# Kernel optimization log

Hardware: AMD Instinct MI355X
Metric: run time of the kernel (lower is better)

The kernel has to match this reference:

```python
import jax, jax.numpy as jnp
import numpy as np

B, T, D, E, I = 4, 2048, 2048, 8, 1024
TOP_K = 2
AUX_COEFF = 0.01


def setup_inputs() -> dict:
    key = jax.random.key(0)
    kx, kg, k1, k3, k2 = jax.random.split(key, 5)
    scale = 0.02
    x = jax.random.normal(kx, (B, T, D), dtype=jnp.float32)
    gate_w = jax.random.normal(kg, (E, D), dtype=jnp.float32) * scale   # nn.Linear weight [out,in]
    w1 = jax.random.normal(k1, (E, I, D), dtype=jnp.float32) * scale    # gate_proj per expert
    w3 = jax.random.normal(k3, (E, I, D), dtype=jnp.float32) * scale    # up_proj per expert
    w2 = jax.random.normal(k2, (E, D, I), dtype=jnp.float32) * scale    # down_proj per expert
    return {"x": x, "gate_w": gate_w, "w1": w1, "w3": w3, "w2": w2}


def reference(x, gate_w, w1, w3, w2):
    b, t, d = x.shape
    e = gate_w.shape[0]
    xf = x.reshape(b * t, d)                                   # [N, D]
    logits = xf @ gate_w.T                                     # [N, E]
    scores = jax.nn.softmax(logits, axis=-1)
    top_scores, top_idx = jax.lax.top_k(scores, TOP_K)         # [N, K]
    top_scores = top_scores / jnp.sum(top_scores, axis=-1, keepdims=True)
    # load-balancing aux loss (Switch Transformer)
    expert_mask = jax.nn.one_hot(top_idx, e, dtype=x.dtype).sum(axis=1)  # [N, E]
    f = expert_mask.mean(axis=0)
    p = scores.mean(axis=0)
    aux_loss = AUX_COEFF * e * jnp.sum(f * p)
    # dense all-expert SwiGLU (matches torch module's dense dispatch)
    h = jax.nn.silu(jnp.einsum('td,eid->tei', xf, w1)) * jnp.einsum('td,eid->tei', xf, w3)  # [N,E,I]
    expert_outs = jnp.einsum('tei,edi->ted', h, w2)            # [N, E, D]
    selected = jnp.take_along_axis(expert_outs, top_idx[:, :, None], axis=1)  # [N, K, D]
    out = jnp.sum(selected * top_scores[:, :, None], axis=1)   # [N, D]
    return out.reshape(b, t, d), aux_loss
```

## Files before the change

### kernel.cpp

```cpp
#include <hip/hip_runtime.h>
#include <hip/hip_bf16.h>

constexpr int kN = 8192;
constexpr int kD = 2048;
constexpr int kE = 8;
constexpr int kI = 1024;

typedef __bf16 bf16x8 __attribute__((ext_vector_type(8)));
typedef float  f32x16 __attribute__((ext_vector_type(16)));

constexpr size_t OFF_COUNTS = 0;
constexpr size_t OFF_PSUM   = 64;
constexpr size_t OFF_OFFS   = 128;
constexpr size_t OFF_CURSOR = 192;
constexpr size_t OFF_TOPE   = 256;
constexpr size_t OFF_TOPW   = OFF_TOPE + (size_t)kN * 8;
constexpr size_t OFF_SLOT   = OFF_TOPW + (size_t)kN * 8;
constexpr size_t OFF_TOK    = OFF_SLOT + (size_t)kN * 8;
constexpr size_t OFF_XG     = OFF_TOK + (size_t)kN * 8;
constexpr size_t OFF_W1B    = OFF_XG  + (size_t)2 * kN * kD * 2;
constexpr size_t OFF_W3B    = OFF_W1B + (size_t)kE * kI * kD * 2;
constexpr size_t OFF_W2B    = OFF_W3B + (size_t)kE * kI * kD * 2;
constexpr size_t OFF_H      = OFF_W2B + (size_t)kE * kD * kI * 2;
constexpr size_t OFF_O2     = OFF_XG;

typedef __attribute__((address_space(1))) const unsigned GU;
typedef __attribute__((address_space(3))) unsigned LU;
__device__ __forceinline__ void gload16(const void* g, void* l) {
    __builtin_amdgcn_global_load_lds((GU*)g, (LU*)l, 16, 0, 0);
}

__global__ __launch_bounds__(256) void convert3_kernel(
    const float* __restrict__ s0, const float* __restrict__ s1,
    const float* __restrict__ s2,
    __bf16* __restrict__ d0, __bf16* __restrict__ d1, __bf16* __restrict__ d2,
    int n8seg)
{
    const int seg = blockIdx.x >> 11;
    const int bid = blockIdx.x & 2047;
    const float* src = (seg == 0) ? s0 : (seg == 1) ? s1 : s2;
    __bf16*      dst = (seg == 0) ? d0 : (seg == 1) ? d1 : d2;
    int i = bid * 256 + threadIdx.x;
    const int stride = 2048 * 256;
    for (; i < n8seg; i += stride) {
        const float4* s = (const float4*)(src + (size_t)i * 8);
        float4 f0 = s[0], f1 = s[1];
        bf16x8 v;
        v[0]=(__bf16)f0.x; v[1]=(__bf16)f0.y; v[2]=(__bf16)f0.z; v[3]=(__bf16)f0.w;
        v[4]=(__bf16)f1.x; v[5]=(__bf16)f1.y; v[6]=(__bf16)f1.z; v[7]=(__bf16)f1.w;
        *(bf16x8*)(dst + (size_t)i * 8) = v;
    }
}

__global__ __launch_bounds__(256) void gate_kernel(
    const float* __restrict__ x, const float* __restrict__ gw,
    unsigned* __restrict__ counts, float* __restrict__ psum,
    int2* __restrict__ tope, float2* __restrict__ topw)
{
    const int tid  = threadIdx.x;
    const int lane = tid & 63;
    const int wv   = tid >> 6;
    const int t    = blockIdx.x * 4 + wv;

    const float* xr = x + (size_t)t * kD;
    float xv[32];
#pragma unroll
    for (int j = 0; j < 32; ++j) xv[j] = xr[lane + 64 * j];

    float s[8];
#pragma unroll
    for (int e = 0; e < 8; ++e) {
        const float* gr = gw + (size_t)e * kD;
        float a = 0.f;
#pragma unroll
        for (int j = 0; j < 32; ++j) a += xv[j] * gr[lane + 64 * j];
        s[e] = a;
    }
#pragma unroll
    for (int off = 32; off > 0; off >>= 1) {
#pragma unroll
        for (int e = 0; e < 8; ++e) s[e] += __shfl_xor(s[e], off, 64);
    }
    float mx = s[0];
#pragma unroll
    for (int e = 1; e < 8; ++e) mx = fmaxf(mx, s[e]);
    float p[8]; float sum = 0.f;
#pragma unroll
    for (int e = 0; e < 8; ++e) { p[e] = expf(s[e] - mx); sum += p[e]; }
    float inv = 1.f / sum;
#pragma unroll
    for (int e = 0; e < 8; ++e) p[e] *= inv;

    int e0 = 0; float p0 = p[0];
#pragma unroll
    for (int e = 1; e < 8; ++e) if (p[e] > p0) { p0 = p[e]; e0 = e; }
    int e1 = -1; float p1 = -1.f;
#pragma unroll
    for (int e = 0; e < 8; ++e) if (e != e0 && p[e] > p1) { p1 = p[e]; e1 = e; }
    float wn = 1.f / (p0 + p1);

    __shared__ float ps[4][8];
    __shared__ unsigned cnt[8];
    if (tid < 8) cnt[tid] = 0u;
    __syncthreads();
    if (lane == 0) {
#pragma unroll
        for (int e = 0; e < 8; ++e) ps[wv][e] = p[e];
        atomicAdd(&cnt[e0], 1u);
        atomicAdd(&cnt[e1], 1u);
        tope[t] = make_int2(e0, e1);
        topw[t] = make_float2(p0 * wn, p1 * wn);
    }
    __syncthreads();
    if (tid < 8) {
        atomicAdd(&psum[tid], ps[0][tid] + ps[1][tid] + ps[2][tid] + ps[3][tid]);
        if (cnt[tid]) atomicAdd(&counts[tid], cnt[tid]);
    }
}

__global__ void scan_kernel(const unsigned* __restrict__ counts,
                            const float* __restrict__ psum,
                            unsigned* __restrict__ offs,
                            unsigned* __restrict__ cursor,
                            float* __restrict__ out)
{
    if (threadIdx.x == 0) {
        unsigned off = 0;
        float a = 0.f;
        for (int e = 0; e < 8; ++e) {
            offs[e] = off; cursor[e] = off; off += counts[e];
            a += ((float)counts[e] / (float)kN) * (psum[e] / (float)kN);
        }
        out[(size_t)kN * kD] = 0.01f * (float)kE * a;
    }
}

__global__ __launch_bounds__(256) void scatter_kernel(
    const int2* __restrict__ tope,
    unsigned* __restrict__ cursor, int* __restrict__ tok,
    int2* __restrict__ slotmap)
{
    int t = blockIdx.x * 256 + threadIdx.x;
    int2 ee = tope[t];
    unsigned q0 = atomicAdd(&cursor[ee.x], 1u);
    tok[q0] = t;
    unsigned q1 = atomicAdd(&cursor[ee.y], 1u);
    tok[q1] = t;
    slotmap[t] = make_int2((int)q0, (int)q1);
}

__global__ __launch_bounds__(256) void gather_kernel(
    const float* __restrict__ x, const int* __restrict__ tok,
    __bf16* __restrict__ Xg)
{
    const int total = 2 * kN * (kD / 8);
    int i = blockIdx.x * 256 + threadIdx.x;
    const int stride = gridDim.x * 256;
    for (; i < total; i += stride) {
        const int slot = i >> 8;
        const int d8   = (i & 255) * 8;
        const float4* s = (const float4*)(x + (size_t)tok[slot] * kD + d8);
        float4 f0 = s[0], f1 = s[1];
        bf16x8 v;
        v[0]=(__bf16)f0.x; v[1]=(__bf16)f0.y; v[2]=(__bf16)f0.z; v[3]=(__bf16)f0.w;
        v[4]=(__bf16)f1.x; v[5]=(__bf16)f1.y; v[6]=(__bf16)f1.z; v[7]=(__bf16)f1.w;
        *(bf16x8*)(Xg + (size_t)slot * kD + d8) = v;
    }
}

__global__ __launch_bounds__(256) void ffn_h_kernel(
    const __bf16* __restrict__ Xg,
    const __bf16* __restrict__ w1b, const __bf16* __restrict__ w3b,
    const unsigned* __restrict__ counts, const unsigned* __restrict__ offs,
    __bf16* __restrict__ H)
{
    const int e  = blockIdx.z;
    const int mt = blockIdx.y;
    const int ct = blockIdx.x;
    const unsigned n_e = counts[e];
    if ((unsigned)(mt * 128) >= n_e) return;
    const unsigned base = offs[e];

    __shared__ __bf16 As[128][64];
    __shared__ __bf16 Bs[128][64];

    const int tid  = threadIdx.x;
    const int lane = tid & 63;
    const int wv   = tid >> 6;
    const int wr   = wv >> 1, wc = wv & 1;

    const __bf16* aptr[4];
    const __bf16* bptr[4];
    __bf16* alds[4];
    __bf16* blds[4];
#pragma unroll
    for (int j = 0; j < 4; ++j) {
        const int r = wv * 32 + j * 8 + (lane >> 3);
        const int c = (((lane & 7) ^ (r & 7)) << 3);
        unsigned grow = (unsigned)(mt * 128 + r);
        grow = grow < n_e ? grow : (n_e - 1);
        aptr[j] = Xg + (size_t)(base + grow) * kD + c;
        alds[j] = &As[wv * 32 + j * 8][0];
        const int rr = r & 63;
        const int h  = ct * 64 + ((r >> 6) << 5) + (rr & 31);
        const __bf16* wsrc = (rr < 32) ? w1b : w3b;
        bptr[j] = wsrc + ((size_t)e * kI + h) * kD + c;
        blds[j] = &Bs[wv * 32 + j * 8][0];
    }

    f32x16 acc[2][2] = {};

    const int ar0 = wr * 64 + (lane & 31);
    const int ar1 = ar0 + 32;
    const int br0 = wc * 64 + (lane & 31);
    const int br1 = br0 + 32;
    const int sgl = lane >> 5;

    for (int k0 = 0; k0 < kD; k0 += 64) {
#pragma unroll
        for (int j = 0; j < 4; ++j) {
            gload16(aptr[j], alds[j]);
            gload16(bptr[j], blds[j]);
            aptr[j] += 64; bptr[j] += 64;
        }
        __syncthreads();

#pragma unroll
        for (int kk = 0; kk < 4; ++kk) {
            const int s = kk * 2 + sgl;
            bf16x8 a0 = *(const bf16x8*)&As[ar0][((s ^ (ar0 & 7)) << 3)];
            bf16x8 a1 = *(const bf16x8*)&As[ar1][((s ^ (ar1 & 7)) << 3)];
            bf16x8 b0 = *(const bf16x8*)&Bs[br0][((s ^ (br0 & 7)) << 3)];
            bf16x8 b1 = *(const bf16x8*)&Bs[br1][((s ^ (br1 & 7)) << 3)];
            acc[0][0] = __builtin_amdgcn_mfma_f32_32x32x16_bf16(a0, b0, acc[0][0], 0, 0, 0);
            acc[0][1] = __builtin_amdgcn_mfma_f32_32x32x16_bf16(a0, b1, acc[0][1], 0, 0, 0);
            acc[1][0] = __builtin_amdgcn_mfma_f32_32x32x16_bf16(a1, b0, acc[1][0], 0, 0, 0);
            acc[1][1] = __builtin_amdgcn_mfma_f32_32x32x16_bf16(a1, b1, acc[1][1], 0, 0, 0);
        }
        __syncthreads();
    }

    const int c0    = lane & 31;
    const int rbase = 4 * (lane >> 5);
    const size_t hcol = (size_t)(ct * 64 + wc * 32 + c0);
#pragma unroll
    for (int m = 0; m < 2; ++m) {
#pragma unroll
        for (int reg = 0; reg < 16; ++reg) {
            const int crow = (reg & 3) + 8 * (reg >> 2) + rbase;
            const unsigned grow = (unsigned)(mt * 128 + wr * 64 + m * 32 + crow);
            if (grow < n_e) {
                float a1 = acc[m][0][reg];
                float a3 = acc[m][1][reg];
                float h = a1 / (1.f + __expf(-a1)) * a3;
                H[(size_t)(base + grow) * kI + hcol] = (__bf16)h;
            }
        }
    }
}

__global__ __launch_bounds__(256) void ffn_out_kernel(
    const __bf16* __restrict__ H, const __bf16* __restrict__ w2b,
    const unsigned* __restrict__ counts, const unsigned* __restrict__ offs,
    __bf16* __restrict__ O2)
{
    const int e  = blockIdx.z;
    const int mt = blockIdx.y;
    const int ct = blockIdx.x;
    const unsigned n_e = counts[e];
    if ((unsigned)(mt * 128) >= n_e) return;
    const unsigned base = offs[e];

    __shared__ __bf16 As[128][64];
    __shared__ __bf16 Bs[128][64];

    const int tid  = threadIdx.x;
    const int lane = tid & 63;
    const int wv   = tid >> 6;
    const int wr   = wv >> 1, wc = wv & 1;

    const __bf16* aptr[4];
    const __bf16* bptr[4];
    __bf16* alds[4];
    __bf16* blds[4];
#pragma unroll
    for (int j = 0; j < 4; ++j) {
        const int r = wv * 32 + j * 8 + (lane >> 3);
        const int c = (((lane & 7) ^ (r & 7)) << 3);
        unsigned grow = (unsigned)(mt * 128 + r);
        grow = grow < n_e ? grow : (n_e - 1);
        aptr[j] = H + (size_t)(base + grow) * kI + c;
        alds[j] = &As[wv * 32 + j * 8][0];
        bptr[j] = w2b + ((size_t)e * kD + ct * 128 + r) * kI + c;
        blds[j] = &Bs[wv * 32 + j * 8][0];
    }

    f32x16 acc[2][2] = {};

    const int ar0 = wr * 64 + (lane & 31);
    const int ar1 = ar0 + 32;
    const int br0 = wc * 64 + (lane & 31);
    const int br1 = br0 + 32;
    const int sgl = lane >> 5;

    for (int k0 = 0; k0 < kI; k0 += 64) {
#pragma unroll
        for (int j = 0; j < 4; ++j) {
            gload16(aptr[j], alds[j]);
            gload16(bptr[j], blds[j]);
            aptr[j] += 64; bptr[j] += 64;
        }
        __syncthreads();

#pragma unroll
        for (int kk = 0; kk < 4; ++kk) {
            const int s = kk * 2 + sgl;
            bf16x8 a0 = *(const bf16x8*)&As[ar0][((s ^ (ar0 & 7)) << 3)];
            bf16x8 a1 = *(const bf16x8*)&As[ar1][((s ^ (ar1 & 7)) << 3)];
            bf16x8 b0 = *(const bf16x8*)&Bs[br0][((s ^ (br0 & 7)) << 3)];
            bf16x8 b1 = *(const bf16x8*)&Bs[br1][((s ^ (br1 & 7)) << 3)];
            acc[0][0] = __builtin_amdgcn_mfma_f32_32x32x16_bf16(a0, b0, acc[0][0], 0, 0, 0);
            acc[0][1] = __builtin_amdgcn_mfma_f32_32x32x16_bf16(a0, b1, acc[0][1], 0, 0, 0);
            acc[1][0] = __builtin_amdgcn_mfma_f32_32x32x16_bf16(a1, b0, acc[1][0], 0, 0, 0);
            acc[1][1] = __builtin_amdgcn_mfma_f32_32x32x16_bf16(a1, b1, acc[1][1], 0, 0, 0);
        }
        __syncthreads();
    }

    const int c0    = lane & 31;
    const int rbase = 4 * (lane >> 5);
#pragma unroll
    for (int m = 0; m < 2; ++m) {
#pragma unroll
        for (int reg = 0; reg < 16; ++reg) {
            const int crow = (reg & 3) + 8 * (reg >> 2) + rbase;
            const unsigned grow = (unsigned)(mt * 128 + wr * 64 + m * 32 + crow);
            if (grow < n_e) {
                __bf16* orow = O2 + (size_t)(base + grow) * kD + ct * 128 + wc * 64 + c0;
                orow[0]  = (__bf16)acc[m][0][reg];
                orow[32] = (__bf16)acc[m][1][reg];
            }
        }
    }
}

__global__ __launch_bounds__(256) void combine_kernel(
    const __bf16* __restrict__ O2, const int2* __restrict__ slotmap,
    const float2* __restrict__ topw, float* __restrict__ out)
{
    const int total = kN * (kD / 8);
    int i = blockIdx.x * 256 + threadIdx.x;
    const int stride = gridDim.x * 256;
    for (; i < total; i += stride) {
        const int t  = i >> 8;
        const int d8 = (i & 255) * 8;
        const int2   sm = slotmap[t];
        const float2 w  = topw[t];
        bf16x8 a = *(const bf16x8*)(O2 + (size_t)sm.x * kD + d8);
        bf16x8 b = *(const bf16x8*)(O2 + (size_t)sm.y * kD + d8);
        float r[8];
#pragma unroll
        for (int j = 0; j < 8; ++j)
            r[j] = w.x * (float)a[j] + w.y * (float)b[j];
        float4* o = (float4*)(out + (size_t)i * 8);
        o[0] = make_float4(r[0], r[1], r[2], r[3]);
        o[1] = make_float4(r[4], r[5], r[6], r[7]);
    }
}

extern "C" void kernel_launch(void* const* d_in, const int* in_sizes, int n_in,
                              void* d_out, int out_size, void* d_ws, size_t ws_size,
                              hipStream_t stream)
{
    const float* x  = (const float*)d_in[0];
    const float* gw = (const float*)d_in[1];
    const float* w1 = (const float*)d_in[2];
    const float* w3 = (const float*)d_in[3];
    const float* w2 = (const float*)d_in[4];
    float* out = (float*)d_out;
    char*  ws  = (char*)d_ws;

    unsigned* counts = (unsigned*)(ws + OFF_COUNTS);
    float*    psum   = (float*)(ws + OFF_PSUM);
    unsigned* offs   = (unsigned*)(ws + OFF_OFFS);
    unsigned* cursor = (unsigned*)(ws + OFF_CURSOR);
    int2*     tope   = (int2*)(ws + OFF_TOPE);
    float2*   topw   = (float2*)(ws + OFF_TOPW);
    int2*     slotmap= (int2*)(ws + OFF_SLOT);
    int*      tok    = (int*)(ws + OFF_TOK);
    __bf16*   Xg     = (__bf16*)(ws + OFF_XG);
    __bf16*   w1b    = (__bf16*)(ws + OFF_W1B);
    __bf16*   w3b    = (__bf16*)(ws + OFF_W3B);
    __bf16*   w2b    = (__bf16*)(ws + OFF_W2B);
    __bf16*   H      = (__bf16*)(ws + OFF_H);
    __bf16*   O2     = (__bf16*)(ws + OFF_O2);

    hipMemsetAsync(d_ws, 0, 256, stream);

    gate_kernel<<<kN / 4, 256, 0, stream>>>(x, gw, counts, psum, tope, topw);
    scan_kernel<<<1, 64, 0, stream>>>(counts, psum, offs, cursor, out);
    scatter_kernel<<<kN / 256, 256, 0, stream>>>(tope, cursor, tok, slotmap);

    convert3_kernel<<<3 * 2048, 256, 0, stream>>>(
        w1, w3, w2, w1b, w3b, w2b, kE * kI * kD / 8);
    gather_kernel<<<2048, 256, 0, stream>>>(x, tok, Xg);

    ffn_h_kernel<<<dim3(kI / 64, 2 * kN / 128, kE), 256, 0, stream>>>(
        Xg, w1b, w3b, counts, offs, H);
    ffn_out_kernel<<<dim3(kD / 128, 2 * kN / 128, kE), 256, 0, stream>>>(
        H, w2b, counts, offs, O2);
    combine_kernel<<<2048, 256, 0, stream>>>(O2, slotmap, topw, out);
}
```

Measured before the change: 471.4 us.

## Fuse token gather into FFN GEMM via row-index indirection, drop gather kernel

```diff
diff --git a/kernel.cpp b/kernel.cpp
--- a/kernel.cpp
+++ b/kernel.cpp
@@ -17,12 +17,12 @@
 constexpr size_t OFF_TOPW   = OFF_TOPE + (size_t)kN * 8;
 constexpr size_t OFF_SLOT   = OFF_TOPW + (size_t)kN * 8;
 constexpr size_t OFF_TOK    = OFF_SLOT + (size_t)kN * 8;
-constexpr size_t OFF_XG     = OFF_TOK + (size_t)kN * 8;
-constexpr size_t OFF_W1B    = OFF_XG  + (size_t)2 * kN * kD * 2;
+constexpr size_t OFF_XB     = OFF_TOK + (size_t)kN * 8;
+constexpr size_t OFF_W1B    = OFF_XB  + (size_t)kN * kD * 2;
 constexpr size_t OFF_W3B    = OFF_W1B + (size_t)kE * kI * kD * 2;
 constexpr size_t OFF_W2B    = OFF_W3B + (size_t)kE * kI * kD * 2;
 constexpr size_t OFF_H      = OFF_W2B + (size_t)kE * kD * kI * 2;
-constexpr size_t OFF_O2     = OFF_XG;
+constexpr size_t OFF_O2     = OFF_W1B;
 
 typedef __attribute__((address_space(1))) const unsigned GU;
 typedef __attribute__((address_space(3))) unsigned LU;
@@ -55,7 +55,8 @@
 __global__ __launch_bounds__(256) void gate_kernel(
     const float* __restrict__ x, const float* __restrict__ gw,
     unsigned* __restrict__ counts, float* __restrict__ psum,
-    int2* __restrict__ tope, float2* __restrict__ topw)
+    int2* __restrict__ tope, float2* __restrict__ topw,
+    __bf16* __restrict__ xb)
 {
     const int tid  = threadIdx.x;
     const int lane = tid & 63;
@@ -66,6 +67,10 @@
     float xv[32];
 #pragma unroll
     for (int j = 0; j < 32; ++j) xv[j] = xr[lane + 64 * j];
+
+    __bf16* xbr = xb + (size_t)t * kD;
+#pragma unroll
+    for (int j = 0; j < 32; ++j) xbr[lane + 64 * j] = (__bf16)xv[j];
 
     float s[8];
 #pragma unroll
@@ -149,30 +154,11 @@
     slotmap[t] = make_int2((int)q0, (int)q1);
 }
 
-__global__ __launch_bounds__(256) void gather_kernel(
-    const float* __restrict__ x, const int* __restrict__ tok,
-    __bf16* __restrict__ Xg)
-{
-    const int total = 2 * kN * (kD / 8);
-    int i = blockIdx.x * 256 + threadIdx.x;
-    const int stride = gridDim.x * 256;
-    for (; i < total; i += stride) {
-        const int slot = i >> 8;
-        const int d8   = (i & 255) * 8;
-        const float4* s = (const float4*)(x + (size_t)tok[slot] * kD + d8);
-        float4 f0 = s[0], f1 = s[1];
-        bf16x8 v;
-        v[0]=(__bf16)f0.x; v[1]=(__bf16)f0.y; v[2]=(__bf16)f0.z; v[3]=(__bf16)f0.w;
-        v[4]=(__bf16)f1.x; v[5]=(__bf16)f1.y; v[6]=(__bf16)f1.z; v[7]=(__bf16)f1.w;
-        *(bf16x8*)(Xg + (size_t)slot * kD + d8) = v;
-    }
-}
-
 __global__ __launch_bounds__(256) void ffn_h_kernel(
-    const __bf16* __restrict__ Xg,
+    const __bf16* __restrict__ xb,
     const __bf16* __restrict__ w1b, const __bf16* __restrict__ w3b,
     const unsigned* __restrict__ counts, const unsigned* __restrict__ offs,
-    __bf16* __restrict__ H)
+    const int* __restrict__ tok, __bf16* __restrict__ H)
 {
     const int e  = blockIdx.z;
     const int mt = blockIdx.y;
@@ -183,12 +169,19 @@
 
     __shared__ __bf16 As[128][64];
     __shared__ __bf16 Bs[128][64];
+    __shared__ int rowtok[128];
 
     const int tid  = threadIdx.x;
     const int lane = tid & 63;
     const int wv   = tid >> 6;
     const int wr   = wv >> 1, wc = wv & 1;
 
+    if (tid < 128) {
+        unsigned r = (unsigned)(mt * 128 + tid);
+        rowtok[tid] = tok[base + (r < n_e ? r : 0u)];
+    }
+    __syncthreads();
+
     const __bf16* aptr[4];
     const __bf16* bptr[4];
     __bf16* alds[4];
@@ -197,9 +190,7 @@
     for (int j = 0; j < 4; ++j) {
         const int r = wv * 32 + j * 8 + (lane >> 3);
         const int c = (((lane & 7) ^ (r & 7)) << 3);
-        unsigned grow = (unsigned)(mt * 128 + r);
-        grow = grow < n_e ? grow : (n_e - 1);
-        aptr[j] = Xg + (size_t)(base + grow) * kD + c;
+        aptr[j] = xb + (size_t)rowtok[r] * kD + c;
         alds[j] = &As[wv * 32 + j * 8][0];
         const int rr = r & 63;
         const int h  = ct * 64 + ((r >> 6) << 5) + (rr & 31);
@@ -388,7 +379,7 @@
     float2*   topw   = (float2*)(ws + OFF_TOPW);
     int2*     slotmap= (int2*)(ws + OFF_SLOT);
     int*      tok    = (int*)(ws + OFF_TOK);
-    __bf16*   Xg     = (__bf16*)(ws + OFF_XG);
+    __bf16*   xb     = (__bf16*)(ws + OFF_XB);
     __bf16*   w1b    = (__bf16*)(ws + OFF_W1B);
     __bf16*   w3b    = (__bf16*)(ws + OFF_W3B);
     __bf16*   w2b    = (__bf16*)(ws + OFF_W2B);
@@ -397,16 +388,15 @@
 
     hipMemsetAsync(d_ws, 0, 256, stream);
 
-    gate_kernel<<<kN / 4, 256, 0, stream>>>(x, gw, counts, psum, tope, topw);
+    gate_kernel<<<kN / 4, 256, 0, stream>>>(x, gw, counts, psum, tope, topw, xb);
     scan_kernel<<<1, 64, 0, stream>>>(counts, psum, offs, cursor, out);
     scatter_kernel<<<kN / 256, 256, 0, stream>>>(tope, cursor, tok, slotmap);
 
     convert3_kernel<<<3 * 2048, 256, 0, stream>>>(
         w1, w3, w2, w1b, w3b, w2b, kE * kI * kD / 8);
-    gather_kernel<<<2048, 256, 0, stream>>>(x, tok, Xg);
 
     ffn_h_kernel<<<dim3(kI / 64, 2 * kN / 128, kE), 256, 0, stream>>>(
-        Xg, w1b, w3b, counts, offs, H);
+        xb, w1b, w3b, counts, offs, tok, H);
     ffn_out_kernel<<<dim3(kD / 128, 2 * kN / 128, kE), 256, 0, stream>>>(
         H, w2b, counts, offs, O2);
     combine_kernel<<<2048, 256, 0, stream>>>(O2, slotmap, topw, out);
```

Result: slower. 511.9 us (+8.6%).

## Compact grouped-GEMM grid via per-expert tile prefix and XCD-aware block remap

Applied to the files above, without the earlier changes.

```diff
diff --git a/kernel.cpp b/kernel.cpp
--- a/kernel.cpp
+++ b/kernel.cpp
@@ -13,11 +13,12 @@
 constexpr size_t OFF_PSUM   = 64;
 constexpr size_t OFF_OFFS   = 128;
 constexpr size_t OFF_CURSOR = 192;
-constexpr size_t OFF_TOPE   = 256;
+constexpr size_t OFF_TBASE  = 256;
+constexpr size_t OFF_TOPE   = 320;
 constexpr size_t OFF_TOPW   = OFF_TOPE + (size_t)kN * 8;
 constexpr size_t OFF_SLOT   = OFF_TOPW + (size_t)kN * 8;
 constexpr size_t OFF_TOK    = OFF_SLOT + (size_t)kN * 8;
-constexpr size_t OFF_XG     = OFF_TOK + (size_t)kN * 8;
+constexpr size_t OFF_XG     = OFF_TOK + (size_t)kN * 8 + 64;
 constexpr size_t OFF_W1B    = OFF_XG  + (size_t)2 * kN * kD * 2;
 constexpr size_t OFF_W3B    = OFF_W1B + (size_t)kE * kI * kD * 2;
 constexpr size_t OFF_W2B    = OFF_W3B + (size_t)kE * kI * kD * 2;
@@ -29,6 +30,9 @@
 __device__ __forceinline__ void gload16(const void* g, void* l) {
     __builtin_amdgcn_global_load_lds((GU*)g, (LU*)l, 16, 0, 0);
 }
+
+constexpr int kMaxTiles = 136;
+constexpr int kGemmGrid = kMaxTiles * 16;
 
 __global__ __launch_bounds__(256) void convert3_kernel(
     const float* __restrict__ s0, const float* __restrict__ s1,
@@ -122,15 +126,18 @@
                             const float* __restrict__ psum,
                             unsigned* __restrict__ offs,
                             unsigned* __restrict__ cursor,
+                            unsigned* __restrict__ tbase,
                             float* __restrict__ out)
 {
     if (threadIdx.x == 0) {
-        unsigned off = 0;
+        unsigned off = 0, tb = 0;
         float a = 0.f;
         for (int e = 0; e < 8; ++e) {
             offs[e] = off; cursor[e] = off; off += counts[e];
+            tbase[e] = tb; tb += (counts[e] + 127u) >> 7;
             a += ((float)counts[e] / (float)kN) * (psum[e] / (float)kN);
         }
+        tbase[8] = tb;
         out[(size_t)kN * kD] = 0.01f * (float)kE * a;
     }
 }
@@ -168,17 +175,30 @@
     }
 }
 
+__device__ __forceinline__ bool gemm_decode(
+    const unsigned* __restrict__ tbase, int& e, int& mt, int& ct)
+{
+    const unsigned w = blockIdx.x;
+    const unsigned orig = (w & 7u) * (kGemmGrid / 8) + (w >> 3);
+    const int tile = (int)(orig >> 4);
+    ct = (int)(orig & 15u);
+    if ((unsigned)tile >= tbase[8]) return false;
+    e = 0;
+#pragma unroll
+    for (int k = 1; k < 8; ++k) if (tbase[k] <= (unsigned)tile) e = k;
+    mt = tile - (int)tbase[e];
+    return true;
+}
+
 __global__ __launch_bounds__(256) void ffn_h_kernel(
     const __bf16* __restrict__ Xg,
     const __bf16* __restrict__ w1b, const __bf16* __restrict__ w3b,
     const unsigned* __restrict__ counts, const unsigned* __restrict__ offs,
-    __bf16* __restrict__ H)
-{
-    const int e  = blockIdx.z;
-    const int mt = blockIdx.y;
-    const int ct = blockIdx.x;
+    const unsigned* __restrict__ tbase, __bf16* __restrict__ H)
+{
+    int e, mt, ct;
+    if (!gemm_decode(tbase, e, mt, ct)) return;
     const unsigned n_e = counts[e];
-    if ((unsigned)(mt * 128) >= n_e) return;
     const unsigned base = offs[e];
 
     __shared__ __bf16 As[128][64];
@@ -262,13 +282,11 @@
 __global__ __launch_bounds__(256) void ffn_out_kernel(
     const __bf16* __restrict__ H, const __bf16* __restrict__ w2b,
     const unsigned* __restrict__ counts, const unsigned* __restrict__ offs,
-    __bf16* __restrict__ O2)
-{
-    const int e  = blockIdx.z;
-    const int mt = blockIdx.y;
-    const int ct = blockIdx.x;
+    const unsigned* __restrict__ tbase, __bf16* __restrict__ O2)
+{
+    int e, mt, ct;
+    if (!gemm_decode(tbase, e, mt, ct)) return;
     const unsigned n_e = counts[e];
-    if ((unsigned)(mt * 128) >= n_e) return;
     const unsigned base = offs[e];
 
     __shared__ __bf16 As[128][64];
@@ -384,6 +402,7 @@
     float*    psum   = (float*)(ws + OFF_PSUM);
     unsigned* offs   = (unsigned*)(ws + OFF_OFFS);
     unsigned* cursor = (unsigned*)(ws + OFF_CURSOR);
+    unsigned* tbase  = (unsigned*)(ws + OFF_TBASE);
     int2*     tope   = (int2*)(ws + OFF_TOPE);
     float2*   topw   = (float2*)(ws + OFF_TOPW);
     int2*     slotmap= (int2*)(ws + OFF_SLOT);
@@ -395,19 +414,19 @@
     __bf16*   H      = (__bf16*)(ws + OFF_H);
     __bf16*   O2     = (__bf16*)(ws + OFF_O2);
 
-    hipMemsetAsync(d_ws, 0, 256, stream);
+    hipMemsetAsync(d_ws, 0, 320, stream);
 
     gate_kernel<<<kN / 4, 256, 0, stream>>>(x, gw, counts, psum, tope, topw);
-    scan_kernel<<<1, 64, 0, stream>>>(counts, psum, offs, cursor, out);
+    scan_kernel<<<1, 64, 0, stream>>>(counts, psum, offs, cursor, tbase, out);
     scatter_kernel<<<kN / 256, 256, 0, stream>>>(tope, cursor, tok, slotmap);
 
     convert3_kernel<<<3 * 2048, 256, 0, stream>>>(
         w1, w3, w2, w1b, w3b, w2b, kE * kI * kD / 8);
     gather_kernel<<<2048, 256, 0, stream>>>(x, tok, Xg);
 
-    ffn_h_kernel<<<dim3(kI / 64, 2 * kN / 128, kE), 256, 0, stream>>>(
-        Xg, w1b, w3b, counts, offs, H);
-    ffn_out_kernel<<<dim3(kD / 128, 2 * kN / 128, kE), 256, 0, stream>>>(
-        H, w2b, counts, offs, O2);
+    ffn_h_kernel<<<kGemmGrid, 256, 0, stream>>>(
+        Xg, w1b, w3b, counts, offs, tbase, H);
+    ffn_out_kernel<<<kGemmGrid, 256, 0, stream>>>(
+        H, w2b, counts, offs, tbase, O2);
     combine_kernel<<<2048, 256, 0, stream>>>(O2, slotmap, topw, out);
 }
```

Measured after the change: 460.6 us (median of 2 runs). 1.02x faster.
